# Kernel tuning notes

Measured on AMD Instinct MI355X. Metric: run time of the kernel, lower is better.

The kernel has to match this reference:

```python
import jax, jax.numpy as jnp
import numpy as np

N = 50000     # nodes
E = 800000    # edges
D_IN = 128
H = 256


def gcn_conv(x, src, dst, W, b, n):
    """PyG GCNConv: add self-loops, symmetric norm, out = A_hat @ (x W) + b."""
    h = x @ W                                   # [n, H_out]
    loop = jnp.arange(n, dtype=src.dtype)
    s = jnp.concatenate([src, loop])            # self-loops appended
    d = jnp.concatenate([dst, loop])
    deg = jnp.zeros((n,), x.dtype).at[d].add(jnp.float32(1.0))
    dinv = jnp.where(deg > 0, jax.lax.rsqrt(deg), 0.0)
    norm = (dinv[s] * dinv[d])[:, None]         # [E+n, 1]
    out = jnp.zeros((n, W.shape[1]), x.dtype).at[d].add(h[s] * norm)
    return out + b


def setup_inputs() -> dict:
    key = jax.random.key(0)
    ks = jax.random.split(key, 12)
    def glorot(k, shp):
        lim = np.sqrt(6.0 / (shp[0] + shp[1]))
        return jax.random.uniform(k, shp, jnp.float32, -lim, lim)
    return {
        "x": jax.random.normal(ks[0], (N, D_IN), jnp.float32),
        "edge_index": jax.random.randint(ks[1], (2, E), 0, N, jnp.int32),
        "enc_W": glorot(ks[2], (D_IN, H)),
        "enc_b": jnp.zeros((H,), jnp.float32),
        "W1": glorot(ks[3], (H, H)),
        "b1": jnp.zeros((H,), jnp.float32),
        "W2": glorot(ks[4], (H, H)),
        "b2": jnp.zeros((H,), jnp.float32),
        "W3": glorot(ks[5], (H, H)),
        "b3": jnp.zeros((H,), jnp.float32),
        "dec_W": glorot(ks[6], (H, 1)),
        "dec_b": jnp.zeros((1,), jnp.float32),
    }


def reference(x, edge_index, enc_W, enc_b, W1, b1, W2, b2, W3, b3, dec_W, dec_b):
    src, dst = edge_index[0], edge_index[1]
    n = x.shape[0]
    h = x @ enc_W + enc_b                       # encoder Linear
    h = gcn_conv(h, src, dst, W1, b1, n)        # model_: conv
    h = jax.nn.relu(h)                          # model_: activation
    h = gcn_conv(h, src, dst, W2, b2, n)        # model_: conv
    h = jax.nn.relu(h)                          # activation after model_
    h = gcn_conv(h, src, dst, W3, b3, n)        # last_layer
    h = jax.nn.relu(h)
    return h @ dec_W + dec_b                    # decoder Linear -> [N, 1]
```

## Files before the change

### kernel.cpp

```cpp
#include <hip/hip_runtime.h>


typedef __attribute__((ext_vector_type(8))) _Float16 half8;
typedef __attribute__((ext_vector_type(4))) _Float16 half4v;
typedef __attribute__((ext_vector_type(4))) float f32x4;

__device__ __forceinline__ void fma4h(float4& acc, float s, const half4v& v) {
  acc.x += s * (float)v.x;
  acc.y += s * (float)v.y;
  acc.z += s * (float)v.z;
  acc.w += s * (float)v.w;
}

__global__ void count_deg_kernel(const int* __restrict__ dst, int* __restrict__ deg, int E) {
  int e = blockIdx.x * blockDim.x + threadIdx.x;
  if (e < E) atomicAdd(&deg[dst[e]], 1);
}

__global__ __launch_bounds__(1024) void scan1_kernel(const int* __restrict__ deg,
                                                     float* __restrict__ dinv,
                                                     int* __restrict__ row_tmp,
                                                     int* __restrict__ bsum, int n) {
  __shared__ int wsum[16];
  int tid = threadIdx.x, lane = tid & 63, wid = tid >> 6;
  int i = blockIdx.x * 1024 + tid;
  int d = (i < n) ? deg[i] + 1 : 0;
  if (i < n) dinv[i] = rsqrtf((float)d);
  int v = d;
  int s = v;
#pragma unroll
  for (int off = 1; off < 64; off <<= 1) {
    int t = __shfl_up(s, off, 64);
    if (lane >= off) s += t;
  }
  if (lane == 63) wsum[wid] = s;
  __syncthreads();
  int wadd = 0;
#pragma unroll
  for (int k = 0; k < 16; ++k) wadd += (k < wid) ? wsum[k] : 0;
  int incl = s + wadd;
  if (i < n) row_tmp[i] = incl - v;
  if (tid == 1023) bsum[blockIdx.x] = incl;
}
__global__ __launch_bounds__(64) void scan2_kernel(const int* __restrict__ bsum,
                                                   int* __restrict__ boff,
                                                   int* __restrict__ row_ptr,
                                                   int n, int nb) {
  int lane = threadIdx.x;
  int v = (lane < nb) ? bsum[lane] : 0;
  int s = v;
#pragma unroll
  for (int off = 1; off < 64; off <<= 1) {
    int t = __shfl_up(s, off, 64);
    if (lane >= off) s += t;
  }
  if (lane < nb) boff[lane] = s - v;
  if (lane == nb - 1) row_ptr[n] = s;
}
__global__ __launch_bounds__(1024) void scan3_kernel(const int* __restrict__ row_tmp,
                                                     const int* __restrict__ boff,
                                                     int* __restrict__ row_ptr,
                                                     int* __restrict__ cursor, int n) {
  int i = blockIdx.x * 1024 + threadIdx.x;
  if (i >= n) return;
  int rp = row_tmp[i] + boff[blockIdx.x];
  row_ptr[i] = rp;
  cursor[i] = rp;
}

__global__ void fill_csr_kernel(const int* __restrict__ src, const int* __restrict__ dst,
                                int* __restrict__ cursor, int* __restrict__ col,
                                int E, int n) {
  int t = blockIdx.x * blockDim.x + threadIdx.x;
  if (t < E) {
    int s = src[t], d = dst[t];
    int pos = atomicAdd(&cursor[d], 1);
    col[pos] = s;
  } else if (t < E + n) {
    int i = t - E;
    int pos = atomicAdd(&cursor[i], 1);
    col[pos] = i;
  }
}

__global__ void prep_kernel(const float* __restrict__ x, _Float16* __restrict__ xh,
                            const float* __restrict__ W0, const float* __restrict__ W1,
                            const float* __restrict__ W2, const float* __restrict__ W3,
                            _Float16* __restrict__ Wt0, _Float16* __restrict__ Wt1,
                            _Float16* __restrict__ Wt2, _Float16* __restrict__ Wt3,
                            int nx4) {
  int t = blockIdx.x * blockDim.x + threadIdx.x;
  if (t < nx4) {
    float4 v = ((const float4*)x)[t];
    half4v h;
    h.x = (_Float16)v.x; h.y = (_Float16)v.y; h.z = (_Float16)v.z; h.w = (_Float16)v.w;
    ((half4v*)xh)[t] = h;
    return;
  }
  int u = t - nx4;
  if (u < 128 * 256) {
    int k = u >> 8, n = u & 255;
    Wt0[(size_t)n * 128 + k] = (_Float16)W0[u];
    return;
  }
  u -= 128 * 256;
  if (u >= 3 * 256 * 256) return;
  int seg = u >> 16;
  int rem = u & 65535;
  int k = rem >> 8, n = rem & 255;
  const float* W = (seg == 0) ? W1 : (seg == 1) ? W2 : W3;
  _Float16* Wt = (seg == 0) ? Wt1 : (seg == 1) ? Wt2 : Wt3;
  Wt[(size_t)n * 256 + k] = (_Float16)W[rem];
}

template<int NCHUNK, int OUTMODE>
__global__ __launch_bounds__(256) void mfma_gemm_kernel(
    const _Float16* __restrict__ A, const _Float16* __restrict__ Bt,
    const float* __restrict__ bias, _Float16* __restrict__ outp, int M) {
  constexpr int K = NCHUNK * 64;
  __shared__ __align__(16) _Float16 As[2 * 128 * 64];
  __shared__ __align__(16) _Float16 Bs[2 * 128 * 64];
  int row0 = (blockIdx.x >> 1) * 128;
  int col0 = (blockIdx.x & 1) * 128;
  int tid = threadIdx.x;
  int w = tid >> 6, l = tid & 63;
  int wm = w >> 1, wn = w & 1;

  f32x4 acc[4][4] = {};

  int srow = l >> 3;
  int sslot = (l & 7) ^ srow;
  int fr_a = wm * 64 + (l & 15);
  int fr_b = wn * 64 + (l & 15);
  int fgrp = l >> 4;

#pragma unroll
  for (int ph = 0; ph < NCHUNK / 2; ++ph) {
#pragma unroll
    for (int c = 0; c < 2; ++c) {
      int kb = (ph * 2 + c) * 64;
#pragma unroll
      for (int q = 0; q < 4; ++q) {
        int r = w * 32 + q * 8 + srow;
        int ga_row = row0 + r; if (ga_row >= M) ga_row = M - 1;
        const _Float16* gA = A + (size_t)ga_row * K + kb + sslot * 8;
        __builtin_amdgcn_global_load_lds(
            (const __attribute__((address_space(1))) void*)gA,
            (__attribute__((address_space(3))) void*)&As[c * 8192 + (w * 32 + q * 8) * 64],
            16, 0, 0);
        const _Float16* gB = Bt + (size_t)(col0 + r) * K + kb + sslot * 8;
        __builtin_amdgcn_global_load_lds(
            (const __attribute__((address_space(1))) void*)gB,
            (__attribute__((address_space(3))) void*)&Bs[c * 8192 + (w * 32 + q * 8) * 64],
            16, 0, 0);
      }
    }
    __syncthreads();
#pragma unroll
    for (int c = 0; c < 2; ++c) {
#pragma unroll
      for (int kk = 0; kk < 2; ++kk) {
        half8 av[4], bv[4];
#pragma unroll
        for (int i = 0; i < 4; ++i) {
          int ra = fr_a + i * 16;
          int sa = (kk * 4 + fgrp) ^ (ra & 7);
          av[i] = *(const half8*)&As[c * 8192 + ra * 64 + sa * 8];
          int rb = fr_b + i * 16;
          int sb = (kk * 4 + fgrp) ^ (rb & 7);
          bv[i] = *(const half8*)&Bs[c * 8192 + rb * 64 + sb * 8];
        }
#pragma unroll
        for (int mi = 0; mi < 4; ++mi)
#pragma unroll
          for (int ni = 0; ni < 4; ++ni)
            acc[mi][ni] = __builtin_amdgcn_mfma_f32_16x16x32_f16(
                av[mi], bv[ni], acc[mi][ni], 0, 0, 0);
      }
    }
    if (ph + 1 < NCHUNK / 2) __syncthreads();
  }

#pragma unroll
  for (int mi = 0; mi < 4; ++mi) {
#pragma unroll
    for (int r = 0; r < 4; ++r) {
      int grow = row0 + wm * 64 + mi * 16 + fgrp * 4 + r;
      if (grow >= M) continue;
#pragma unroll
      for (int ni = 0; ni < 4; ++ni) {
        int gcol = col0 + wn * 64 + ni * 16 + (l & 15);
        float v = acc[mi][ni][r];
        if (OUTMODE == 1) v += bias[gcol];
        outp[(size_t)grow * 256 + gcol] = (_Float16)v;
      }
    }
  }
}

template<bool DECODE>
__global__ __launch_bounds__(256) void aggregate_kernel(
    const _Float16* __restrict__ tmp, const int* __restrict__ row_ptr,
    const int* __restrict__ col, const float* __restrict__ dinv,
    const float* __restrict__ bias, _Float16* __restrict__ hout,
    const float* __restrict__ decW, const float* __restrict__ decb,
    float* __restrict__ out, int n) {
  int wave = threadIdx.x >> 6;
  int lane = threadIdx.x & 63;
  int node = blockIdx.x * 4 + wave;
  if (node >= n) return;
  const half4v* tmp4 = (const half4v*)tmp;
  float dn = dinv[node];
  float4 a0 = ((const float4*)bias)[lane];
  float4 a1 = make_float4(0.f, 0.f, 0.f, 0.f);
  float4 a2 = make_float4(0.f, 0.f, 0.f, 0.f);
  float4 a3 = make_float4(0.f, 0.f, 0.f, 0.f);
  int p = row_ptr[node], end = row_ptr[node + 1];

  for (; p + 8 <= end; p += 8) {
    int j0 = col[p + 0], j1 = col[p + 1], j2 = col[p + 2], j3 = col[p + 3];
    int j4 = col[p + 4], j5 = col[p + 5], j6 = col[p + 6], j7 = col[p + 7];
    float w0 = dinv[j0] * dn, w1 = dinv[j1] * dn, w2 = dinv[j2] * dn, w3 = dinv[j3] * dn;
    float w4 = dinv[j4] * dn, w5 = dinv[j5] * dn, w6 = dinv[j6] * dn, w7 = dinv[j7] * dn;
    half4v v0 = tmp4[(size_t)j0 * 64 + lane];
    half4v v1 = tmp4[(size_t)j1 * 64 + lane];
    half4v v2 = tmp4[(size_t)j2 * 64 + lane];
    half4v v3 = tmp4[(size_t)j3 * 64 + lane];
    half4v v4 = tmp4[(size_t)j4 * 64 + lane];
    half4v v5 = tmp4[(size_t)j5 * 64 + lane];
    half4v v6 = tmp4[(size_t)j6 * 64 + lane];
    half4v v7 = tmp4[(size_t)j7 * 64 + lane];
    fma4h(a0, w0, v0); fma4h(a1, w1, v1); fma4h(a2, w2, v2); fma4h(a3, w3, v3);
    fma4h(a0, w4, v4); fma4h(a1, w5, v5); fma4h(a2, w6, v6); fma4h(a3, w7, v7);
  }
  for (; p + 4 <= end; p += 4) {
    int j0 = col[p + 0], j1 = col[p + 1], j2 = col[p + 2], j3 = col[p + 3];
    float w0 = dinv[j0] * dn, w1 = dinv[j1] * dn, w2 = dinv[j2] * dn, w3 = dinv[j3] * dn;
    half4v v0 = tmp4[(size_t)j0 * 64 + lane];
    half4v v1 = tmp4[(size_t)j1 * 64 + lane];
    half4v v2 = tmp4[(size_t)j2 * 64 + lane];
    half4v v3 = tmp4[(size_t)j3 * 64 + lane];
    fma4h(a0, w0, v0); fma4h(a1, w1, v1); fma4h(a2, w2, v2); fma4h(a3, w3, v3);
  }
  for (; p < end; ++p) {
    int j = col[p];
    float s = dinv[j] * dn;
    half4v v = tmp4[(size_t)j * 64 + lane];
    fma4h(a0, s, v);
  }
  float4 acc;
  acc.x = fmaxf(a0.x + a1.x + a2.x + a3.x, 0.f);
  acc.y = fmaxf(a0.y + a1.y + a2.y + a3.y, 0.f);
  acc.z = fmaxf(a0.z + a1.z + a2.z + a3.z, 0.f);
  acc.w = fmaxf(a0.w + a1.w + a2.w + a3.w, 0.f);

  if (!DECODE) {
    half4v hv;
    hv.x = (_Float16)acc.x; hv.y = (_Float16)acc.y;
    hv.z = (_Float16)acc.z; hv.w = (_Float16)acc.w;
    ((half4v*)hout)[(size_t)node * 64 + lane] = hv;
  } else {
    float4 w = ((const float4*)decW)[lane];
    float s = acc.x * w.x + acc.y * w.y + acc.z * w.z + acc.w * w.w;
#pragma unroll
    for (int off = 32; off > 0; off >>= 1) s += __shfl_xor(s, off);
    if (lane == 0) out[node] = s + decb[0];
  }
}


extern "C" void kernel_launch(void* const* d_in, const int* in_sizes, int n_in,
                              void* d_out, int out_size, void* d_ws, size_t ws_size,
                              hipStream_t stream) {
  const float* x      = (const float*)d_in[0];
  const int*   eidx   = (const int*)d_in[1];
  const float* enc_W  = (const float*)d_in[2];
  const float* enc_b  = (const float*)d_in[3];
  const float* W1     = (const float*)d_in[4];
  const float* b1     = (const float*)d_in[5];
  const float* W2     = (const float*)d_in[6];
  const float* b2     = (const float*)d_in[7];
  const float* W3     = (const float*)d_in[8];
  const float* b3     = (const float*)d_in[9];
  const float* dec_W  = (const float*)d_in[10];
  const float* dec_b  = (const float*)d_in[11];
  float* out = (float*)d_out;

  const int D_IN = 128;
  const int N = in_sizes[0] / D_IN;
  const int E = in_sizes[1] / 2;
  const int* src = eidx;
  const int* dst = eidx + E;

  _Float16* h    = (_Float16*)d_ws;
  _Float16* tmp  = h + (size_t)N * 256;
  _Float16* xh   = tmp + (size_t)N * 256;
  _Float16* WtE  = xh + (size_t)N * 128;
  _Float16* Wt1  = WtE + 256 * 128;
  _Float16* Wt2  = Wt1 + 256 * 256;
  _Float16* Wt3  = Wt2 + 256 * 256;
  int*   deg     = (int*)(Wt3 + 256 * 256);
  float* dinv    = (float*)(deg + N);
  int*   row_ptr = (int*)(dinv + N);
  int*   row_tmp = row_ptr + (N + 1);
  int*   cursor  = row_tmp + N;
  int*   bsum    = cursor + N;
  int*   boff    = bsum + 64;
  int*   col     = boff + 64;

  dim3 blk(256);
  dim3 gE((E + 255) / 256);
  dim3 gEN((E + N + 255) / 256);
  int nb = (N + 1023) / 1024;
  int nx4 = N * 32;

  hipMemsetAsync(deg, 0, (size_t)N * 4, stream);
  count_deg_kernel<<<gE, blk, 0, stream>>>(dst, deg, E);
  scan1_kernel<<<nb, 1024, 0, stream>>>(deg, dinv, row_tmp, bsum, N);
  scan2_kernel<<<1, 64, 0, stream>>>(bsum, boff, row_ptr, N, nb);
  scan3_kernel<<<nb, 1024, 0, stream>>>(row_tmp, boff, row_ptr, cursor, N);
  fill_csr_kernel<<<gEN, blk, 0, stream>>>(src, dst, cursor, col, E, N);

  int prep_threads = nx4 + 128 * 256 + 3 * 256 * 256;
  prep_kernel<<<(prep_threads + 255) / 256, blk, 0, stream>>>(
      x, xh, enc_W, W1, W2, W3, WtE, Wt1, Wt2, Wt3, nx4);

  dim3 gemm_grid(((N + 127) / 128) * 2);
  dim3 agg_grid((N + 3) / 4);

  mfma_gemm_kernel<2, 1><<<gemm_grid, blk, 0, stream>>>(xh, WtE, enc_b, h, N);
  mfma_gemm_kernel<4, 0><<<gemm_grid, blk, 0, stream>>>(h, Wt1, nullptr, tmp, N);
  aggregate_kernel<false><<<agg_grid, blk, 0, stream>>>(tmp, row_ptr, col, dinv, b1, h,
                                                        nullptr, nullptr, nullptr, N);
  mfma_gemm_kernel<4, 0><<<gemm_grid, blk, 0, stream>>>(h, Wt2, nullptr, tmp, N);
  aggregate_kernel<false><<<agg_grid, blk, 0, stream>>>(tmp, row_ptr, col, dinv, b2, h,
                                                        nullptr, nullptr, nullptr, N);
  mfma_gemm_kernel<4, 0><<<gemm_grid, blk, 0, stream>>>(h, Wt3, nullptr, tmp, N);
  aggregate_kernel<true><<<agg_grid, blk, 0, stream>>>(tmp, row_ptr, col, dinv, b3, nullptr,
                                                       dec_W, dec_b, out, N);
}
```

Before: 350.7 us.

## Fold encoder into first GCN weight and aggregate raw 128-wide input first

The encoder Linear and the first GCN weight are merged into one 128x256 matrix (encW·W1) plus a bias vector (enc_b·W1), computed on device each call. The first layer now aggregates the 128-wide fp16 input over the graph, together with a per-node normalized degree sum, and then runs a single K=128 GEMM. That GEMM's epilogue adds the degree-scaled bias term, b1 and ReLU. This removes one full 256-wide GEMM, and the first aggregation gathers half as many bytes per edge. The cost is a small serial matrix-product kernel and a different fp16 rounding order.

```diff
diff --git a/kernel.cpp b/kernel.cpp
--- a/kernel.cpp
+++ b/kernel.cpp
@@ -84,9 +84,7 @@
 }
 
 __global__ void prep_kernel(const float* __restrict__ x, _Float16* __restrict__ xh,
-                            const float* __restrict__ W0, const float* __restrict__ W1,
                             const float* __restrict__ W2, const float* __restrict__ W3,
-                            _Float16* __restrict__ Wt0, _Float16* __restrict__ Wt1,
                             _Float16* __restrict__ Wt2, _Float16* __restrict__ Wt3,
                             int nx4) {
   int t = blockIdx.x * blockDim.x + threadIdx.x;
@@ -98,25 +96,92 @@
     return;
   }
   int u = t - nx4;
-  if (u < 128 * 256) {
-    int k = u >> 8, n = u & 255;
-    Wt0[(size_t)n * 128 + k] = (_Float16)W0[u];
-    return;
-  }
-  u -= 128 * 256;
-  if (u >= 3 * 256 * 256) return;
+  if (u >= 2 * 256 * 256) return;
   int seg = u >> 16;
   int rem = u & 65535;
   int k = rem >> 8, n = rem & 255;
-  const float* W = (seg == 0) ? W1 : (seg == 1) ? W2 : W3;
-  _Float16* Wt = (seg == 0) ? Wt1 : (seg == 1) ? Wt2 : Wt3;
+  const float* W = (seg == 0) ? W2 : W3;
+  _Float16* Wt = (seg == 0) ? Wt2 : Wt3;
   Wt[(size_t)n * 256 + k] = (_Float16)W[rem];
+}
+
+__global__ __launch_bounds__(256) void wf_kernel(const float* __restrict__ encW,
+                                                 const float* __restrict__ enc_b,
+                                                 const float* __restrict__ W1,
+                                                 _Float16* __restrict__ Wtf,
+                                                 float* __restrict__ cvec) {
+  int k = blockIdx.x;
+  int nn = threadIdx.x;
+  float s = 0.f;
+  if (k < 128) {
+    for (int m = 0; m < 256; ++m)
+      s += encW[k * 256 + m] * W1[m * 256 + nn];
+    Wtf[(size_t)nn * 128 + k] = (_Float16)s;
+  } else {
+    for (int m = 0; m < 256; ++m)
+      s += enc_b[m] * W1[m * 256 + nn];
+    cvec[nn] = s;
+  }
+}
+
+__global__ __launch_bounds__(256) void aggregate_x_kernel(
+    const _Float16* __restrict__ xh, const int* __restrict__ row_ptr,
+    const int* __restrict__ col, const float* __restrict__ dinv,
+    _Float16* __restrict__ a1, float* __restrict__ rs, int n) {
+  int grp = threadIdx.x >> 5;
+  int gl = threadIdx.x & 31;
+  int node = blockIdx.x * 8 + grp;
+  if (node >= n) return;
+  const half4v* x4 = (const half4v*)xh;
+  float dn = dinv[node];
+  float4 a0 = make_float4(0.f, 0.f, 0.f, 0.f);
+  float4 b0 = make_float4(0.f, 0.f, 0.f, 0.f);
+  float4 c0 = make_float4(0.f, 0.f, 0.f, 0.f);
+  float4 e0 = make_float4(0.f, 0.f, 0.f, 0.f);
+  float dsum = 0.f;
+  int p = row_ptr[node], end = row_ptr[node + 1];
+
+  for (; p + 8 <= end; p += 8) {
+    int j0 = col[p + 0], j1 = col[p + 1], j2 = col[p + 2], j3 = col[p + 3];
+    int j4 = col[p + 4], j5 = col[p + 5], j6 = col[p + 6], j7 = col[p + 7];
+    float d0 = dinv[j0], d1 = dinv[j1], d2 = dinv[j2], d3 = dinv[j3];
+    float d4 = dinv[j4], d5 = dinv[j5], d6 = dinv[j6], d7 = dinv[j7];
+    half4v v0 = x4[(size_t)j0 * 32 + gl];
+    half4v v1 = x4[(size_t)j1 * 32 + gl];
+    half4v v2 = x4[(size_t)j2 * 32 + gl];
+    half4v v3 = x4[(size_t)j3 * 32 + gl];
+    half4v v4 = x4[(size_t)j4 * 32 + gl];
+    half4v v5 = x4[(size_t)j5 * 32 + gl];
+    half4v v6 = x4[(size_t)j6 * 32 + gl];
+    half4v v7 = x4[(size_t)j7 * 32 + gl];
+    fma4h(a0, d0, v0); fma4h(b0, d1, v1); fma4h(c0, d2, v2); fma4h(e0, d3, v3);
+    fma4h(a0, d4, v4); fma4h(b0, d5, v5); fma4h(c0, d6, v6); fma4h(e0, d7, v7);
+    dsum += ((d0 + d1) + (d2 + d3)) + ((d4 + d5) + (d6 + d7));
+  }
+  for (; p < end; ++p) {
+    int j = col[p];
+    float d = dinv[j];
+    half4v v = x4[(size_t)j * 32 + gl];
+    fma4h(a0, d, v);
+    dsum += d;
+  }
+  float4 acc;
+  acc.x = (a0.x + b0.x + c0.x + e0.x) * dn;
+  acc.y = (a0.y + b0.y + c0.y + e0.y) * dn;
+  acc.z = (a0.z + b0.z + c0.z + e0.z) * dn;
+  acc.w = (a0.w + b0.w + c0.w + e0.w) * dn;
+  half4v hv;
+  hv.x = (_Float16)acc.x; hv.y = (_Float16)acc.y;
+  hv.z = (_Float16)acc.z; hv.w = (_Float16)acc.w;
+  ((half4v*)a1)[(size_t)node * 32 + gl] = hv;
+  if (gl == 0) rs[node] = dsum * dn;
 }
 
 template<int NCHUNK, int OUTMODE>
 __global__ __launch_bounds__(256) void mfma_gemm_kernel(
     const _Float16* __restrict__ A, const _Float16* __restrict__ Bt,
-    const float* __restrict__ bias, _Float16* __restrict__ outp, int M) {
+    const float* __restrict__ bias, const float* __restrict__ rs,
+    const float* __restrict__ cvec, _Float16* __restrict__ outp, int M) {
   constexpr int K = NCHUNK * 64;
   __shared__ __align__(16) _Float16 As[2 * 128 * 64];
   __shared__ __align__(16) _Float16 Bs[2 * 128 * 64];
@@ -187,11 +252,15 @@
     for (int r = 0; r < 4; ++r) {
       int grow = row0 + wm * 64 + mi * 16 + fgrp * 4 + r;
       if (grow >= M) continue;
+      float rsv = (OUTMODE == 2) ? rs[grow] : 0.f;
 #pragma unroll
       for (int ni = 0; ni < 4; ++ni) {
         int gcol = col0 + wn * 64 + ni * 16 + (l & 15);
         float v = acc[mi][ni][r];
-        if (OUTMODE == 1) v += bias[gcol];
+        if (OUTMODE == 2) {
+          v += rsv * cvec[gcol] + bias[gcol];
+          v = fmaxf(v, 0.f);
+        }
         outp[(size_t)grow * 256 + gcol] = (_Float16)v;
       }
     }
@@ -295,11 +364,13 @@
   _Float16* h    = (_Float16*)d_ws;
   _Float16* tmp  = h + (size_t)N * 256;
   _Float16* xh   = tmp + (size_t)N * 256;
-  _Float16* WtE  = xh + (size_t)N * 128;
-  _Float16* Wt1  = WtE + 256 * 128;
-  _Float16* Wt2  = Wt1 + 256 * 256;
+  _Float16* a1   = xh + (size_t)N * 128;
+  _Float16* Wtf  = a1 + (size_t)N * 128;
+  _Float16* Wt2  = Wtf + 256 * 128;
   _Float16* Wt3  = Wt2 + 256 * 256;
-  int*   deg     = (int*)(Wt3 + 256 * 256);
+  float* cvec    = (float*)(Wt3 + 256 * 256);
+  float* rs      = cvec + 256;
+  int*   deg     = (int*)(rs + N);
   float* dinv    = (float*)(deg + N);
   int*   row_ptr = (int*)(dinv + N);
   int*   row_tmp = row_ptr + (N + 1);
@@ -321,21 +392,21 @@
   scan3_kernel<<<nb, 1024, 0, stream>>>(row_tmp, boff, row_ptr, cursor, N);
   fill_csr_kernel<<<gEN, blk, 0, stream>>>(src, dst, cursor, col, E, N);
 
-  int prep_threads = nx4 + 128 * 256 + 3 * 256 * 256;
+  int prep_threads = nx4 + 2 * 256 * 256;
   prep_kernel<<<(prep_threads + 255) / 256, blk, 0, stream>>>(
-      x, xh, enc_W, W1, W2, W3, WtE, Wt1, Wt2, Wt3, nx4);
+      x, xh, W2, W3, Wt2, Wt3, nx4);
+  wf_kernel<<<129, blk, 0, stream>>>(enc_W, enc_b, W1, Wtf, cvec);
 
   dim3 gemm_grid(((N + 127) / 128) * 2);
   dim3 agg_grid((N + 3) / 4);
-
-  mfma_gemm_kernel<2, 1><<<gemm_grid, blk, 0, stream>>>(xh, WtE, enc_b, h, N);
-  mfma_gemm_kernel<4, 0><<<gemm_grid, blk, 0, stream>>>(h, Wt1, nullptr, tmp, N);
-  aggregate_kernel<false><<<agg_grid, blk, 0, stream>>>(tmp, row_ptr, col, dinv, b1, h,
-                                                        nullptr, nullptr, nullptr, N);
-  mfma_gemm_kernel<4, 0><<<gemm_grid, blk, 0, stream>>>(h, Wt2, nullptr, tmp, N);
+  dim3 aggx_grid((N + 7) / 8);
+
+  aggregate_x_kernel<<<aggx_grid, blk, 0, stream>>>(xh, row_ptr, col, dinv, a1, rs, N);
+  mfma_gemm_kernel<2, 2><<<gemm_grid, blk, 0, stream>>>(a1, Wtf, b1, rs, cvec, h, N);
+  mfma_gemm_kernel<4, 0><<<gemm_grid, blk, 0, stream>>>(h, Wt2, nullptr, nullptr, nullptr, tmp, N);
   aggregate_kernel<false><<<agg_grid, blk, 0, stream>>>(tmp, row_ptr, col, dinv, b2, h,
                                                         nullptr, nullptr, nullptr, N);
-  mfma_gemm_kernel<4, 0><<<gemm_grid, blk, 0, stream>>>(h, Wt3, nullptr, tmp, N);
+  mfma_gemm_kernel<4, 0><<<gemm_grid, blk, 0, stream>>>(h, Wt3, nullptr, nullptr, nullptr, tmp, N);
   aggregate_kernel<true><<<agg_grid, blk, 0, stream>>>(tmp, row_ptr, col, dinv, b3, nullptr,
                                                        dec_W, dec_b, out, N);
 }
```

Result: faster. 333.8 us (-4.8%).
